# Performance work log

Measured on AMD Instinct MI355X. Metric: run time of the kernel, lower is better.

## Reference

```python
import jax, jax.numpy as jnp
import numpy as np

BITS = 8
BOUND = 2.0 ** (BITS - 1) - 1.0  # 127, symmetric int8 bound
EPS = 1e-6


def fake_quant(x, scale):
    """Symmetric fake quantization with straight-through estimator."""
    q = jnp.clip(jnp.round(x * scale), -BOUND, BOUND) / scale
    return x + jax.lax.stop_gradient(q - x)


def dense_aqt(x, w, b, mask):
    """AQT-style quantized dense: per-tensor input scale (masked stats),
    per-output-channel weight scale, int8-range fake quant, float GEMM.
    x: [N, Cin], w: [Cin, Cout], b: [Cout], mask: [N, 1]."""
    x_max = jnp.max(jnp.abs(x * mask))                       # masked per-tensor stat
    sx = BOUND / jnp.maximum(x_max, EPS)
    w_max = jnp.max(jnp.abs(w), axis=0, keepdims=True)        # [1, Cout]
    sw = BOUND / jnp.maximum(w_max, EPS)
    xq = fake_quant(x, sx)
    wq = fake_quant(w, sw)
    return jnp.matmul(xq, wq) + b


def setup_inputs() -> dict:
    key = jax.random.key(0)
    k1, k2, k3 = jax.random.split(key, 3)
    B, S, C, H = 4, 2048, 1024, 4096
    inputs = jax.random.normal(k1, (B, S, C), dtype=jnp.float32)
    padding_mask = jnp.ones((B, S, 1), dtype=jnp.float32)
    W1 = jax.random.normal(k2, (C, H), dtype=jnp.float32) * (1.0 / np.sqrt(C))
    b1 = jnp.zeros((H,), dtype=jnp.float32)
    W2 = jax.random.normal(k3, (H, C), dtype=jnp.float32) * (1.0 / np.sqrt(H))
    b2 = jnp.zeros((C,), dtype=jnp.float32)
    return {"inputs": inputs, "padding_mask": padding_mask,
            "W1": W1, "b1": b1, "W2": W2, "b2": b2}


def reference(inputs, padding_mask, W1, b1, W2, b2):
    B, S, C = inputs.shape
    x = inputs.reshape(B * S, C)
    m = padding_mask.reshape(B * S, 1)
    h = jax.nn.relu(dense_aqt(x, W1, b1, m))   # dropout is no-op (deterministic)
    out = dense_aqt(h, W2, b2, m)              # dropout is no-op (deterministic)
    return out.reshape(B, S, C)
```

## Files before the change

### kernel.cpp

```cpp
#include <hip/hip_runtime.h>
#include <hip/hip_fp16.h>
#include <stdint.h>


#define EPSQ 1e-6f
typedef int v4i __attribute__((ext_vector_type(4)));
typedef int v16i __attribute__((ext_vector_type(16)));

__device__ __forceinline__ int8_t quant1(float x, float s) {
  return (int8_t)(int)fminf(fmaxf(rintf(x * s), -127.f), 127.f);
}
__device__ __forceinline__ void async16(const int8_t* g, int8_t* l) {
  __builtin_amdgcn_global_load_lds(
      (const __attribute__((address_space(1))) void*)g,
      (__attribute__((address_space(3))) void*)l, 16, 0, 0);
}
__device__ __forceinline__ unsigned short f2h(float f) {
  __half h = __float2half(f);
  return *(unsigned short*)&h;
}
__device__ __forceinline__ float h2f(unsigned short u) {
  __half h = *(__half*)&u;
  return __half2float(h);
}
__device__ __forceinline__ float4 max4(float4 m, float4 v) {
  m.x = fmaxf(m.x, fabsf(v.x)); m.y = fmaxf(m.y, fabsf(v.y));
  m.z = fmaxf(m.z, fabsf(v.z)); m.w = fmaxf(m.w, fabsf(v.w));
  return m;
}

__global__ __launch_bounds__(256) void k_stats(
    const float* __restrict__ x, const float* __restrict__ mask,
    const float* __restrict__ W1, const float* __restrict__ W2,
    float* __restrict__ pmaxX, float* __restrict__ pcm1, float* __restrict__ pcm2) {
  const int bx = blockIdx.x, tid = threadIdx.x;
  if (bx < 64) {
    const int sp = bx & 15, cg = bx >> 4;
    const int col = cg * 1024 + tid * 4;
    float4 m = {0.f, 0.f, 0.f, 0.f};
#pragma unroll 8
    for (int r = 0; r < 64; ++r)
      m = max4(m, *(const float4*)(W1 + (size_t)(sp * 64 + r) * 4096 + col));
    *(float4*)(pcm1 + sp * 4096 + col) = m;
  } else if (bx < 128) {
    const int sp = bx - 64;
    const int col = tid * 4;
    float4 m = {0.f, 0.f, 0.f, 0.f};
#pragma unroll 8
    for (int r = 0; r < 64; ++r)
      m = max4(m, *(const float4*)(W2 + (size_t)(sp * 64 + r) * 1024 + col));
    *(float4*)(pcm2 + sp * 1024 + col) = m;
  } else {
    __shared__ float red[4];
    const int b = bx - 128;
    float lmax = 0.f;
    for (int c = b * 256 + tid; c < 1048576; c += 262144) {
      size_t idx = (size_t)c * 8;
      float mk = fabsf(mask[idx >> 10]);
      float4 m4 = {0.f, 0.f, 0.f, 0.f};
      m4 = max4(m4, *(const float4*)(x + idx));
      m4 = max4(m4, *(const float4*)(x + idx + 4));
      lmax = fmaxf(lmax, fmaxf(fmaxf(m4.x, m4.y), fmaxf(m4.z, m4.w)) * mk);
    }
    for (int s = 32; s; s >>= 1) lmax = fmaxf(lmax, __shfl_down(lmax, s));
    if ((tid & 63) == 0) red[tid >> 6] = lmax;
    __syncthreads();
    if (tid == 0)
      pmaxX[b] = fmaxf(fmaxf(red[0], red[1]), fmaxf(red[2], red[3]));
  }
}

__global__ __launch_bounds__(256) void k_quant(
    const float* __restrict__ x, const float* __restrict__ W1, const float* __restrict__ W2,
    const float* __restrict__ pmaxX, const float* __restrict__ pcm1, const float* __restrict__ pcm2,
    int8_t* __restrict__ qx, int8_t* __restrict__ qw1, int8_t* __restrict__ qw2,
    float* __restrict__ cm1, float* __restrict__ cm2, float* __restrict__ scG) {
  const int bx = blockIdx.x, tid = threadIdx.x;
  if (bx < 2048) {
    __shared__ float red[4];
    float v = fmaxf(fmaxf(pmaxX[tid], pmaxX[tid + 256]),
                    fmaxf(pmaxX[tid + 512], pmaxX[tid + 768]));
    for (int s = 32; s; s >>= 1) v = fmaxf(v, __shfl_down(v, s));
    if ((tid & 63) == 0) red[tid >> 6] = v;
    __syncthreads();
    const float xmax = fmaxf(fmaxf(red[0], red[1]), fmaxf(red[2], red[3]));
    if (bx == 0 && tid == 0) scG[0] = xmax;
    const float s = 127.0f / fmaxf(xmax, EPSQ);
    const int wave = tid >> 6, lane = tid & 63;
    const int f = bx * 4 + wave;
    const int r = (f >> 5) * 32 + (lane & 31);
    const int k = (f & 31) * 32 + (lane >> 5) * 16;
    const float4* src = (const float4*)(x + (size_t)r * 1024 + k);
    union { int8_t p[16]; uint4 v; } u;
#pragma unroll
    for (int i = 0; i < 4; ++i) {
      float4 fv = src[i];
      u.p[4 * i] = quant1(fv.x, s);     u.p[4 * i + 1] = quant1(fv.y, s);
      u.p[4 * i + 2] = quant1(fv.z, s); u.p[4 * i + 3] = quant1(fv.w, s);
    }
    *(uint4*)(qx + (size_t)f * 1024 + lane * 16) = u.v;
  } else if (bx < 2304) {
    int id = (bx - 2048) * 256 + tid;
    int n4 = id & 1023, kc = id >> 10;
    const int col = n4 * 4;
    float4 cm = {0.f, 0.f, 0.f, 0.f};
#pragma unroll
    for (int sp = 0; sp < 16; ++sp) {
      float4 p = *(const float4*)(pcm1 + sp * 4096 + col);
      cm.x = fmaxf(cm.x, p.x); cm.y = fmaxf(cm.y, p.y);
      cm.z = fmaxf(cm.z, p.z); cm.w = fmaxf(cm.w, p.w);
    }
    if (kc == 0) *(float4*)(cm1 + col) = cm;
    const float s0 = 127.0f / fmaxf(cm.x, EPSQ), s1 = 127.0f / fmaxf(cm.y, EPSQ);
    const float s2 = 127.0f / fmaxf(cm.z, EPSQ), s3 = 127.0f / fmaxf(cm.w, EPSQ);
    union { int8_t p[16]; uint4 v; } u0, u1, u2, u3;
#pragma unroll
    for (int j = 0; j < 16; ++j) {
      float4 f = *(const float4*)(W1 + (size_t)(kc * 16 + j) * 4096 + col);
      u0.p[j] = quant1(f.x, s0); u1.p[j] = quant1(f.y, s1);
      u2.p[j] = quant1(f.z, s2); u3.p[j] = quant1(f.w, s3);
    }
    int8_t* base = qw1 + ((size_t)(col >> 5) * 32 + (kc >> 1)) * 1024 +
                   (kc & 1) * 512 + (col & 31) * 16;
    *(uint4*)(base) = u0.v;      *(uint4*)(base + 16) = u1.v;
    *(uint4*)(base + 32) = u2.v; *(uint4*)(base + 48) = u3.v;
  } else {
    int id = (bx - 2304) * 256 + tid;
    int n4 = id & 255, kc = id >> 8;
    const int col = n4 * 4;
    float4 cm = {0.f, 0.f, 0.f, 0.f};
#pragma unroll
    for (int sp = 0; sp < 64; ++sp) {
      float4 p = *(const float4*)(pcm2 + sp * 1024 + col);
      cm.x = fmaxf(cm.x, p.x); cm.y = fmaxf(cm.y, p.y);
      cm.z = fmaxf(cm.z, p.z); cm.w = fmaxf(cm.w, p.w);
    }
    if (kc == 0) *(float4*)(cm2 + col) = cm;
    const float s0 = 127.0f / fmaxf(cm.x, EPSQ), s1 = 127.0f / fmaxf(cm.y, EPSQ);
    const float s2 = 127.0f / fmaxf(cm.z, EPSQ), s3 = 127.0f / fmaxf(cm.w, EPSQ);
    union { int8_t p[16]; uint4 v; } u0, u1, u2, u3;
#pragma unroll
    for (int j = 0; j < 16; ++j) {
      float4 f = *(const float4*)(W2 + (size_t)(kc * 16 + j) * 1024 + col);
      u0.p[j] = quant1(f.x, s0); u1.p[j] = quant1(f.y, s1);
      u2.p[j] = quant1(f.z, s2); u3.p[j] = quant1(f.w, s3);
    }
    int8_t* base = qw2 + ((size_t)(col >> 5) * 128 + (kc >> 1)) * 1024 +
                   (kc & 1) * 512 + (col & 31) * 16;
    *(uint4*)(base) = u0.v;      *(uint4*)(base + 16) = u1.v;
    *(uint4*)(base + 32) = u2.v; *(uint4*)(base + 48) = u3.v;
  }
}

template <int MODE, int KF, int WPE>
__global__ __launch_bounds__(256, WPE) void gemm_i8(
    const int8_t* __restrict__ A, const int8_t* __restrict__ Bt,
    const float* __restrict__ sxp, const float* __restrict__ cmax,
    const float* __restrict__ bias, const float* __restrict__ mask,
    void* __restrict__ outp, float* __restrict__ pmaxH, int M, int N, int K) {
  __shared__ __align__(16) int8_t lsA[2][KF * 4096];
  __shared__ __align__(16) int8_t lsB[2][KF * 4096];
  __shared__ float red[4];
  const int tid = threadIdx.x;
  const int wave = tid >> 6, lane = tid & 63;
  const int m0 = blockIdx.x * 128, n0 = blockIdx.y * 128;
  const int wm = (wave & 1) * 64, wn = (wave >> 1) * 64;
  const int Kf = K >> 5;

  v16i acc[2][2] = {};

  const int8_t* gA[KF]; const int8_t* gB[KF];
  int8_t* dA[KF]; int8_t* dB[KF];
#pragma unroll
  for (int kc = 0; kc < KF; ++kc) {
    gA[kc] = A + ((size_t)((m0 >> 5) + wave) * Kf + kc) * 1024 + lane * 16;
    gB[kc] = Bt + ((size_t)((n0 >> 5) + wave) * Kf + kc) * 1024 + lane * 16;
    dA[kc] = lsA[0] + (kc * 4 + wave) * 1024 + lane * 16;
    dB[kc] = lsB[0] + (kc * 4 + wave) * 1024 + lane * 16;
  }

  const int nsteps = K / (32 * KF);
#pragma unroll
  for (int kc = 0; kc < KF; ++kc) { async16(gA[kc], dA[kc]); async16(gB[kc], dB[kc]); }

  const int mI = (wave & 1) * 2;
  const int nI = (wave >> 1) * 2;

  for (int kb = 0; kb < nsteps; ++kb) {
    const int cur = kb & 1;
    const int co = cur * (KF * 4096);
    __syncthreads();
    if (kb + 1 < nsteps) {
      const size_t ko = (size_t)(kb + 1) * (KF * 1024);
      const int po = (cur ^ 1) * (KF * 4096);
#pragma unroll
      for (int kc = 0; kc < KF; ++kc) {
        async16(gA[kc] + ko, dA[kc] + po);
        async16(gB[kc] + ko, dB[kc] + po);
      }
    }
#pragma unroll
    for (int kc = 0; kc < KF; ++kc) {
      v4i af[2], bf[2];
#pragma unroll
      for (int mt = 0; mt < 2; ++mt)
        af[mt] = *(const v4i*)(lsA[0] + co + (kc * 4 + mI + mt) * 1024 + lane * 16);
#pragma unroll
      for (int nt = 0; nt < 2; ++nt)
        bf[nt] = *(const v4i*)(lsB[0] + co + (kc * 4 + nI + nt) * 1024 + lane * 16);
#pragma unroll
      for (int mt = 0; mt < 2; ++mt)
#pragma unroll
        for (int nt = 0; nt < 2; ++nt)
          acc[mt][nt] = __builtin_amdgcn_mfma_i32_32x32x32_i8(af[mt], bf[nt], acc[mt][nt], 0, 0, 0);
    }
  }

  const float asc = fmaxf(sxp[0], EPSQ) * (1.0f / 127.0f);
  const int cl = lane & 31;
  const int rbase = 4 * (lane >> 5);

  float bsc[2], bv[2];
#pragma unroll
  for (int nt = 0; nt < 2; ++nt) {
    int col = n0 + wn + nt * 32 + cl;
    bsc[nt] = fmaxf(cmax[col], EPSQ) * (1.0f / 127.0f) * asc;
    bv[nt] = bias[col];
  }

  if (MODE == 0) {
    unsigned short* hO = (unsigned short*)outp;
    float lmax = 0.f;
#pragma unroll
    for (int mt = 0; mt < 2; ++mt)
#pragma unroll
      for (int g = 0; g < 4; ++g)
#pragma unroll
        for (int r2 = 0; r2 < 4; ++r2) {
          int row = m0 + wm + mt * 32 + g * 8 + r2 + rbase;
          float mk = fabsf(mask[row]);
          unsigned short* orow = hO + (size_t)row * N + n0 + wn + cl;
#pragma unroll
          for (int nt = 0; nt < 2; ++nt) {
            float v = (float)acc[mt][nt][g * 4 + r2] * bsc[nt] + bv[nt];
            v = fmaxf(v, 0.f);
            orow[nt * 32] = f2h(v);
            lmax = fmaxf(lmax, v * mk);
          }
        }
    for (int s = 32; s; s >>= 1) lmax = fmaxf(lmax, __shfl_down(lmax, s));
    if (lane == 0) red[wave] = lmax;
    __syncthreads();
    if (tid == 0)
      pmaxH[blockIdx.x * gridDim.y + blockIdx.y] =
          fmaxf(fmaxf(red[0], red[1]), fmaxf(red[2], red[3]));
  } else {
    float* oO = (float*)outp;
#pragma unroll
    for (int mt = 0; mt < 2; ++mt)
#pragma unroll
      for (int g = 0; g < 4; ++g)
#pragma unroll
        for (int r2 = 0; r2 < 4; ++r2) {
          int row = m0 + wm + mt * 32 + g * 8 + r2 + rbase;
          float* orow = oO + (size_t)row * N + n0 + wn + cl;
#pragma unroll
          for (int nt = 0; nt < 2; ++nt)
            orow[nt * 32] = (float)acc[mt][nt][g * 4 + r2] * bsc[nt] + bv[nt];
        }
  }
}

__global__ __launch_bounds__(256) void k_quant_h(
    const unsigned short* __restrict__ h, const float* __restrict__ pmaxH,
    float* __restrict__ scG, int8_t* __restrict__ q) {
  __shared__ float red[4];
  const int tid = threadIdx.x;
  float v = 0.f;
#pragma unroll
  for (int j = 0; j < 8; ++j) v = fmaxf(v, pmaxH[tid + 256 * j]);
  for (int s = 32; s; s >>= 1) v = fmaxf(v, __shfl_down(v, s));
  if ((tid & 63) == 0) red[tid >> 6] = v;
  __syncthreads();
  const float hmax = fmaxf(fmaxf(red[0], red[1]), fmaxf(red[2], red[3]));
  if (blockIdx.x == 0 && tid == 0) scG[1] = hmax;
  const float s = 127.0f / fmaxf(hmax, EPSQ);
  const int wave = tid >> 6, lane = tid & 63;
  const int f = blockIdx.x * 4 + wave;
  const int r = (f >> 7) * 32 + (lane & 31);
  const int k = (f & 127) * 32 + (lane >> 5) * 16;
  const uint4* hp = (const uint4*)(h + (size_t)r * 4096 + k);
  union { uint4 v; unsigned short s[8]; } a, b;
  a.v = hp[0];
  b.v = hp[1];
  union { int8_t p[16]; uint4 v; } u;
#pragma unroll
  for (int i = 0; i < 8; ++i) {
    u.p[i] = quant1(h2f(a.s[i]), s);
    u.p[i + 8] = quant1(h2f(b.s[i]), s);
  }
  *(uint4*)(q + (size_t)f * 1024 + lane * 16) = u.v;
}

extern "C" void kernel_launch(void* const* d_in, const int* in_sizes, int n_in,
                              void* d_out, int out_size, void* d_ws, size_t ws_size,
                              hipStream_t stream) {
  const float* x  = (const float*)d_in[0];
  const float* mk = (const float*)d_in[1];
  const float* W1 = (const float*)d_in[2];
  const float* b1 = (const float*)d_in[3];
  const float* W2 = (const float*)d_in[4];
  const float* b2 = (const float*)d_in[5];
  float* out = (float*)d_out;

  float* scG   = (float*)d_ws;
  float* pmaxX = scG + 8;
  float* pmaxH = pmaxX + 1024;
  float* pcm1  = pmaxH + 2048;
  float* pcm2  = pcm1 + 65536;
  float* cm1   = pcm2 + 65536;
  float* cm2   = cm1 + 4096;
  int8_t* qx  = (int8_t*)(cm2 + 1024);
  int8_t* qw1 = qx  + (size_t)8192 * 1024;
  int8_t* qw2 = qw1 + (size_t)4096 * 1024;
  int8_t* qh  = qw2 + (size_t)1024 * 4096;
  unsigned short* h = (unsigned short*)(qh + (size_t)8192 * 4096);

  k_stats<<<1152, 256, 0, stream>>>(x, mk, W1, W2, pmaxX, pcm1, pcm2);
  k_quant<<<2560, 256, 0, stream>>>(x, W1, W2, pmaxX, pcm1, pcm2,
                                    qx, qw1, qw2, cm1, cm2, scG);
  gemm_i8<0, 2, 5><<<dim3(64, 32), 256, 0, stream>>>(
      qx, qw1, scG, cm1, b1, mk, (void*)h, pmaxH, 8192, 4096, 1024);
  k_quant_h<<<8192, 256, 0, stream>>>(h, pmaxH, scG, qh);
  gemm_i8<1, 4, 2><<<dim3(64, 8), 256, 0, stream>>>(
      qh, qw2, scG + 1, cm2, b2, mk, (void*)out, nullptr, 8192, 1024, 4096);
}
```

Baseline: 250.3 us.

## Fuse hidden-activation quantization into second GEMM's A-tile loader

Removes the separate k_quant_h pass and the int8 hidden buffer. The first GEMM now writes its fp16 hidden output directly in the MFMA fragment layout. The second GEMM reduces the per-block maxima itself, then loads fp16 fragments through registers, quantizes them and stores them to LDS, prefetching one step ahead. This saves a kernel launch and a full read and write of the int8 activation, but the A loads in GEMM2 are no longer asynchronous LDS loads. Each GEMM2 block also re-reduces the 2048 partial maxima and re-quantizes the same A tiles that the other column blocks quantize.

```diff
diff --git a/kernel.cpp b/kernel.cpp
--- a/kernel.cpp
+++ b/kernel.cpp
@@ -152,12 +152,12 @@
   }
 }
 
-template <int MODE, int KF, int WPE>
-__global__ __launch_bounds__(256, WPE) void gemm_i8(
+__global__ __launch_bounds__(256, 5) void gemm1(
     const int8_t* __restrict__ A, const int8_t* __restrict__ Bt,
     const float* __restrict__ sxp, const float* __restrict__ cmax,
     const float* __restrict__ bias, const float* __restrict__ mask,
-    void* __restrict__ outp, float* __restrict__ pmaxH, int M, int N, int K) {
+    unsigned short* __restrict__ hfrag, float* __restrict__ pmaxH) {
+  constexpr int KF = 2, Kf = 32;
   __shared__ __align__(16) int8_t lsA[2][KF * 4096];
   __shared__ __align__(16) int8_t lsB[2][KF * 4096];
   __shared__ float red[4];
@@ -165,7 +165,6 @@
   const int wave = tid >> 6, lane = tid & 63;
   const int m0 = blockIdx.x * 128, n0 = blockIdx.y * 128;
   const int wm = (wave & 1) * 64, wn = (wave >> 1) * 64;
-  const int Kf = K >> 5;
 
   v16i acc[2][2] = {};
 
@@ -179,12 +178,11 @@
     dB[kc] = lsB[0] + (kc * 4 + wave) * 1024 + lane * 16;
   }
 
-  const int nsteps = K / (32 * KF);
+  const int nsteps = 1024 / (32 * KF);
 #pragma unroll
   for (int kc = 0; kc < KF; ++kc) { async16(gA[kc], dA[kc]); async16(gB[kc], dB[kc]); }
 
-  const int mI = (wave & 1) * 2;
-  const int nI = (wave >> 1) * 2;
+  const int mI = (wave & 1) * 2, nI = (wave >> 1) * 2;
 
   for (int kb = 0; kb < nsteps; ++kb) {
     const int cur = kb & 1;
@@ -228,78 +226,158 @@
     bv[nt] = bias[col];
   }
 
-  if (MODE == 0) {
-    unsigned short* hO = (unsigned short*)outp;
-    float lmax = 0.f;
-#pragma unroll
-    for (int mt = 0; mt < 2; ++mt)
-#pragma unroll
-      for (int g = 0; g < 4; ++g)
-#pragma unroll
-        for (int r2 = 0; r2 < 4; ++r2) {
-          int row = m0 + wm + mt * 32 + g * 8 + r2 + rbase;
-          float mk = fabsf(mask[row]);
-          unsigned short* orow = hO + (size_t)row * N + n0 + wn + cl;
-#pragma unroll
-          for (int nt = 0; nt < 2; ++nt) {
-            float v = (float)acc[mt][nt][g * 4 + r2] * bsc[nt] + bv[nt];
-            v = fmaxf(v, 0.f);
-            orow[nt * 32] = f2h(v);
-            lmax = fmaxf(lmax, v * mk);
-          }
+  const int hwoff = (cl >> 4) * 512 + (cl & 15);
+  float lmax = 0.f;
+#pragma unroll
+  for (int mt = 0; mt < 2; ++mt) {
+    const size_t rowblk = (size_t)((m0 + wm) >> 5) + mt;
+#pragma unroll
+    for (int g = 0; g < 4; ++g)
+#pragma unroll
+      for (int r2 = 0; r2 < 4; ++r2) {
+        const int rloc = g * 8 + r2 + rbase;
+        const int row = m0 + wm + mt * 32 + rloc;
+        const float mk = fabsf(mask[row]);
+#pragma unroll
+        for (int nt = 0; nt < 2; ++nt) {
+          const size_t kblk = (size_t)((n0 + wn) >> 5) + nt;
+          float v = (float)acc[mt][nt][g * 4 + r2] * bsc[nt] + bv[nt];
+          v = fmaxf(v, 0.f);
+          hfrag[(rowblk * 128 + kblk) * 1024 + hwoff + rloc * 16] = f2h(v);
+          lmax = fmaxf(lmax, v * mk);
         }
-    for (int s = 32; s; s >>= 1) lmax = fmaxf(lmax, __shfl_down(lmax, s));
-    if (lane == 0) red[wave] = lmax;
-    __syncthreads();
-    if (tid == 0)
-      pmaxH[blockIdx.x * gridDim.y + blockIdx.y] =
-          fmaxf(fmaxf(red[0], red[1]), fmaxf(red[2], red[3]));
-  } else {
-    float* oO = (float*)outp;
-#pragma unroll
-    for (int mt = 0; mt < 2; ++mt)
-#pragma unroll
-      for (int g = 0; g < 4; ++g)
-#pragma unroll
-        for (int r2 = 0; r2 < 4; ++r2) {
-          int row = m0 + wm + mt * 32 + g * 8 + r2 + rbase;
-          float* orow = oO + (size_t)row * N + n0 + wn + cl;
-#pragma unroll
-          for (int nt = 0; nt < 2; ++nt)
-            orow[nt * 32] = (float)acc[mt][nt][g * 4 + r2] * bsc[nt] + bv[nt];
-        }
-  }
-}
-
-__global__ __launch_bounds__(256) void k_quant_h(
-    const unsigned short* __restrict__ h, const float* __restrict__ pmaxH,
-    float* __restrict__ scG, int8_t* __restrict__ q) {
+      }
+  }
+  for (int s = 32; s; s >>= 1) lmax = fmaxf(lmax, __shfl_down(lmax, s));
+  if (lane == 0) red[wave] = lmax;
+  __syncthreads();
+  if (tid == 0)
+    pmaxH[blockIdx.x * gridDim.y + blockIdx.y] =
+        fmaxf(fmaxf(red[0], red[1]), fmaxf(red[2], red[3]));
+}
+
+__global__ __launch_bounds__(256, 2) void gemm2(
+    const unsigned short* __restrict__ hfrag, const int8_t* __restrict__ Bt,
+    const float* __restrict__ pmaxH, const float* __restrict__ cmax,
+    const float* __restrict__ bias, float* __restrict__ out) {
+  constexpr int KF = 4, Kf = 128;
+  __shared__ __align__(16) int8_t lsA[2][KF * 4096];
+  __shared__ __align__(16) int8_t lsB[2][KF * 4096];
   __shared__ float red[4];
   const int tid = threadIdx.x;
+  const int wave = tid >> 6, lane = tid & 63;
+
   float v = 0.f;
 #pragma unroll
   for (int j = 0; j < 8; ++j) v = fmaxf(v, pmaxH[tid + 256 * j]);
   for (int s = 32; s; s >>= 1) v = fmaxf(v, __shfl_down(v, s));
-  if ((tid & 63) == 0) red[tid >> 6] = v;
+  if (lane == 0) red[wave] = v;
   __syncthreads();
   const float hmax = fmaxf(fmaxf(red[0], red[1]), fmaxf(red[2], red[3]));
-  if (blockIdx.x == 0 && tid == 0) scG[1] = hmax;
-  const float s = 127.0f / fmaxf(hmax, EPSQ);
-  const int wave = tid >> 6, lane = tid & 63;
-  const int f = blockIdx.x * 4 + wave;
-  const int r = (f >> 7) * 32 + (lane & 31);
-  const int k = (f & 127) * 32 + (lane >> 5) * 16;
-  const uint4* hp = (const uint4*)(h + (size_t)r * 4096 + k);
-  union { uint4 v; unsigned short s[8]; } a, b;
-  a.v = hp[0];
-  b.v = hp[1];
-  union { int8_t p[16]; uint4 v; } u;
-#pragma unroll
-  for (int i = 0; i < 8; ++i) {
-    u.p[i] = quant1(h2f(a.s[i]), s);
-    u.p[i + 8] = quant1(h2f(b.s[i]), s);
-  }
-  *(uint4*)(q + (size_t)f * 1024 + lane * 16) = u.v;
+  const float sq = 127.0f / fmaxf(hmax, EPSQ);
+  const float asc = fmaxf(hmax, EPSQ) * (1.0f / 127.0f);
+
+  const int m0 = blockIdx.x * 128, n0 = blockIdx.y * 128;
+  const int wm = (wave & 1) * 64, wn = (wave >> 1) * 64;
+
+  v16i acc[2][2] = {};
+
+  const uint4* hA = (const uint4*)hfrag;
+  size_t aIdx[KF]; const int8_t* gB[KF]; int8_t* dA[KF]; int8_t* dB[KF];
+#pragma unroll
+  for (int kc = 0; kc < KF; ++kc) {
+    aIdx[kc] = ((size_t)((m0 >> 5) + wave) * Kf + kc) * 128 + lane * 2;
+    gB[kc] = Bt + ((size_t)((n0 >> 5) + wave) * Kf + kc) * 1024 + lane * 16;
+    dA[kc] = lsA[0] + (kc * 4 + wave) * 1024 + lane * 16;
+    dB[kc] = lsB[0] + (kc * 4 + wave) * 1024 + lane * 16;
+  }
+
+  const int nsteps = 4096 / (32 * KF);
+#pragma unroll
+  for (int kc = 0; kc < KF; ++kc) {
+    uint4 a = hA[aIdx[kc]], b = hA[aIdx[kc] + 1];
+    const unsigned short* as = (const unsigned short*)&a;
+    const unsigned short* bs = (const unsigned short*)&b;
+    union { int8_t p[16]; v4i q; } u;
+#pragma unroll
+    for (int i = 0; i < 8; ++i) {
+      u.p[i] = quant1(h2f(as[i]), sq);
+      u.p[i + 8] = quant1(h2f(bs[i]), sq);
+    }
+    *(v4i*)dA[kc] = u.q;
+    async16(gB[kc], dB[kc]);
+  }
+
+  const int mI = (wave & 1) * 2, nI = (wave >> 1) * 2;
+
+  for (int kb = 0; kb < nsteps; ++kb) {
+    const int cur = kb & 1;
+    const int co = cur * (KF * 4096);
+    __syncthreads();
+    uint4 pa[KF], pb[KF];
+    const bool more = (kb + 1 < nsteps);
+    const int po = (cur ^ 1) * (KF * 4096);
+    if (more) {
+#pragma unroll
+      for (int kc = 0; kc < KF; ++kc) {
+        const size_t ai = aIdx[kc] + (size_t)(kb + 1) * (KF * 128);
+        pa[kc] = hA[ai];
+        pb[kc] = hA[ai + 1];
+        async16(gB[kc] + (size_t)(kb + 1) * (KF * 1024), dB[kc] + po);
+      }
+    }
+#pragma unroll
+    for (int kc = 0; kc < KF; ++kc) {
+      v4i af[2], bf[2];
+#pragma unroll
+      for (int mt = 0; mt < 2; ++mt)
+        af[mt] = *(const v4i*)(lsA[0] + co + (kc * 4 + mI + mt) * 1024 + lane * 16);
+#pragma unroll
+      for (int nt = 0; nt < 2; ++nt)
+        bf[nt] = *(const v4i*)(lsB[0] + co + (kc * 4 + nI + nt) * 1024 + lane * 16);
+#pragma unroll
+      for (int mt = 0; mt < 2; ++mt)
+#pragma unroll
+        for (int nt = 0; nt < 2; ++nt)
+          acc[mt][nt] = __builtin_amdgcn_mfma_i32_32x32x32_i8(af[mt], bf[nt], acc[mt][nt], 0, 0, 0);
+    }
+    if (more) {
+#pragma unroll
+      for (int kc = 0; kc < KF; ++kc) {
+        const unsigned short* as = (const unsigned short*)&pa[kc];
+        const unsigned short* bs = (const unsigned short*)&pb[kc];
+        union { int8_t p[16]; v4i q; } u;
+#pragma unroll
+        for (int i = 0; i < 8; ++i) {
+          u.p[i] = quant1(h2f(as[i]), sq);
+          u.p[i + 8] = quant1(h2f(bs[i]), sq);
+        }
+        *(v4i*)(dA[kc] + po) = u.q;
+      }
+    }
+  }
+
+  const int cl = lane & 31;
+  const int rbase = 4 * (lane >> 5);
+  float bsc[2], bv[2];
+#pragma unroll
+  for (int nt = 0; nt < 2; ++nt) {
+    int col = n0 + wn + nt * 32 + cl;
+    bsc[nt] = fmaxf(cmax[col], EPSQ) * (1.0f / 127.0f) * asc;
+    bv[nt] = bias[col];
+  }
+#pragma unroll
+  for (int mt = 0; mt < 2; ++mt)
+#pragma unroll
+    for (int g = 0; g < 4; ++g)
+#pragma unroll
+      for (int r2 = 0; r2 < 4; ++r2) {
+        int row = m0 + wm + mt * 32 + g * 8 + r2 + rbase;
+        float* orow = out + (size_t)row * 1024 + n0 + wn + cl;
+#pragma unroll
+        for (int nt = 0; nt < 2; ++nt)
+          orow[nt * 32] = (float)acc[mt][nt][g * 4 + r2] * bsc[nt] + bv[nt];
+      }
 }
 
 extern "C" void kernel_launch(void* const* d_in, const int* in_sizes, int n_in,
@@ -323,15 +401,11 @@
   int8_t* qx  = (int8_t*)(cm2 + 1024);
   int8_t* qw1 = qx  + (size_t)8192 * 1024;
   int8_t* qw2 = qw1 + (size_t)4096 * 1024;
-  int8_t* qh  = qw2 + (size_t)1024 * 4096;
-  unsigned short* h = (unsigned short*)(qh + (size_t)8192 * 4096);
+  unsigned short* h = (unsigned short*)(qw2 + (size_t)1024 * 4096);
 
   k_stats<<<1152, 256, 0, stream>>>(x, mk, W1, W2, pmaxX, pcm1, pcm2);
   k_quant<<<2560, 256, 0, stream>>>(x, W1, W2, pmaxX, pcm1, pcm2,
                                     qx, qw1, qw2, cm1, cm2, scG);
-  gemm_i8<0, 2, 5><<<dim3(64, 32), 256, 0, stream>>>(
-      qx, qw1, scG, cm1, b1, mk, (void*)h, pmaxH, 8192, 4096, 1024);
-  k_quant_h<<<8192, 256, 0, stream>>>(h, pmaxH, scG, qh);
-  gemm_i8<1, 4, 2><<<dim3(64, 8), 256, 0, stream>>>(
-      qh, qw2, scG + 1, cm2, b2, mk, (void*)out, nullptr, 8192, 1024, 4096);
-}
+  gemm1<<<dim3(64, 32), 256, 0, stream>>>(qx, qw1, scG, cm1, b1, mk, h, pmaxH);
+  gemm2<<<dim3(64, 8), 256, 0, stream>>>(h, qw2, pmaxH, cm2, b2, out);
+}
```

After: 262.3 us. 1.05x slower.
